# Performance work log

Hardware: AMD Instinct MI355X
Metric: run time of the kernel (lower is better)

## Reference

```python
import jax, jax.numpy as jnp
import numpy as np

WS = 4           # window size (cubic)
NUM_HEADS = 4
DIM = 128
NW = 392         # number of windows per sample
B = 8            # batch
N = WS ** 3      # 64 tokens per window


def _relative_position_index(ws):
    coords = np.stack(np.meshgrid(np.arange(ws), np.arange(ws), np.arange(ws), indexing='ij'))  # [3,ws,ws,ws]
    flat = coords.reshape(3, -1)                      # [3, ws^3]
    rel = flat[:, :, None] - flat[:, None, :]         # [3, N, N]
    rel = rel.transpose(1, 2, 0).copy()               # [N, N, 3]
    rel += ws - 1
    rel[:, :, 0] *= (2 * ws - 1) ** 2
    rel[:, :, 1] *= (2 * ws - 1)
    return rel.sum(-1)                                # [N, N] int


def setup_inputs() -> dict:
    key = jax.random.key(0)
    ks = jax.random.split(key, 8)
    B_ = NW * B
    x = jax.random.normal(ks[0], (B_, N, DIM), dtype=jnp.float32)
    mask = jax.random.normal(ks[1], (NW, N, N), dtype=jnp.float32)
    # learned params
    qkv_w = jax.random.normal(ks[2], (3 * DIM, DIM), dtype=jnp.float32) * 0.02
    qkv_b = jnp.zeros((3 * DIM,), dtype=jnp.float32)
    proj_w = jax.random.normal(ks[3], (DIM, DIM), dtype=jnp.float32) * 0.02
    proj_b = jnp.zeros((DIM,), dtype=jnp.float32)
    tbl = jax.random.normal(ks[4], ((2 * WS - 1) ** 3, NUM_HEADS), dtype=jnp.float32) * 0.02
    rel_index = jnp.asarray(_relative_position_index(WS), dtype=jnp.int32)  # [N, N]
    return {"x": x, "mask": mask, "qkv_w": qkv_w, "qkv_b": qkv_b,
            "proj_w": proj_w, "proj_b": proj_b, "rpb_table": tbl,
            "rel_index": rel_index}


def reference(x, mask, qkv_w, qkv_b, proj_w, proj_b, rpb_table, rel_index):
    B_, N_, C = x.shape
    H = NUM_HEADS
    hd = C // H
    scale = hd ** (-0.5)
    # qkv projection: [B_, N, 3, H, hd] -> (3, B_, H, N, hd)
    qkv = (x @ qkv_w.T + qkv_b).reshape(B_, N_, 3, H, hd).transpose(2, 0, 3, 1, 4)
    q, k, v = qkv[0], qkv[1], qkv[2]
    attn = jnp.einsum('bhnd,bhmd->bhnm', q * scale, k)        # [B_, H, N, N]
    # gathered relative position bias: [N, N, H] -> [H, N, N]
    rpe = rpb_table[rel_index].transpose(2, 0, 1)
    attn = attn + rpe[None]
    nW = mask.shape[0]
    attn = attn.reshape(B_ // nW, nW, H, N_, N_) + mask[None, :, None]
    attn = attn.reshape(B_, H, N_, N_)
    attn = jax.nn.softmax(attn, axis=-1)
    out = jnp.einsum('bhnm,bhmd->bnhd', attn, v).reshape(B_, N_, C)
    return out @ proj_w.T + proj_b
```

## Files before the change

### kernel.cpp

```cpp
#include <hip/hip_runtime.h>
#include <hip/hip_bf16.h>


typedef __bf16 bf16x8 __attribute__((ext_vector_type(8)));
typedef __bf16 bf16x4 __attribute__((ext_vector_type(4)));
typedef float f32x4 __attribute__((ext_vector_type(4)));

#define NWMASK 392
#define SCALE 0.17677669529663687f

__global__ void prep(const float* __restrict__ qkv_w, const float* __restrict__ proj_w,
                     const float* __restrict__ tbl, const int* __restrict__ ridx,
                     __bf16* __restrict__ wqkv, __bf16* __restrict__ wproj,
                     float* __restrict__ rpe) {
    int i = blockIdx.x * 256 + threadIdx.x;
    if (i < 49152) {
        wqkv[i] = (__bf16)qkv_w[i];
    } else if (i < 65536) {
        int j = i - 49152;  wproj[j] = (__bf16)proj_w[j];
    } else {
        int j = i - 65536;
        rpe[j] = tbl[ridx[j & 4095] * 4 + (j >> 12)];
    }
}

__global__ __launch_bounds__(256, 4) void wattn_main(
    const float* __restrict__ x, const float* __restrict__ mask,
    const float* __restrict__ qkv_b, const float* __restrict__ proj_b,
    const __bf16* __restrict__ wqkv, const __bf16* __restrict__ wproj,
    const float* __restrict__ rpe, float* __restrict__ out)
{
    __shared__ __align__(16) __bf16 smem[18944];
    const int win  = blockIdx.x;
    const int tid  = threadIdx.x;
    const int h    = tid >> 6;
    const int lane = tid & 63;
    const int quad = lane >> 4;
    const int l16  = lane & 15;

    __bf16* const xs  = smem;
    __bf16* const buf = smem + 8704 + h * 2560;

    {
        const float* xb = x + (size_t)win * 8192;
        #pragma unroll
        for (int i = 0; i < 2; ++i) {
            const int row  = h * 16 + (lane >> 3) + i * 8;
            const int colg = (lane & 7) * 16;
            const float* xp = xb + row * 128 + colg;
            float4 a0 = *(const float4*)(xp);
            float4 a1 = *(const float4*)(xp + 4);
            float4 a2 = *(const float4*)(xp + 8);
            float4 a3 = *(const float4*)(xp + 12);
            bf16x8 t0, t1;
            t0[0]=(__bf16)a0.x; t0[1]=(__bf16)a0.y; t0[2]=(__bf16)a0.z; t0[3]=(__bf16)a0.w;
            t0[4]=(__bf16)a1.x; t0[5]=(__bf16)a1.y; t0[6]=(__bf16)a1.z; t0[7]=(__bf16)a1.w;
            t1[0]=(__bf16)a2.x; t1[1]=(__bf16)a2.y; t1[2]=(__bf16)a2.z; t1[3]=(__bf16)a2.w;
            t1[4]=(__bf16)a3.x; t1[5]=(__bf16)a3.y; t1[6]=(__bf16)a3.z; t1[7]=(__bf16)a3.w;
            *(bf16x8*)(xs + row * 136 + colg)     = t0;
            *(bf16x8*)(xs + row * 136 + colg + 8) = t1;
        }
    }

    bf16x8 kwf[2][4]; float kbb[2];
    #pragma unroll
    for (int nt = 0; nt < 2; ++nt) {
        const int ng = 128 + h * 32 + nt * 16 + l16;
        kbb[nt] = qkv_b[ng];
        #pragma unroll
        for (int kt = 0; kt < 4; ++kt)
            kwf[nt][kt] = *(const bf16x8*)(wqkv + ng * 128 + kt * 32 + quad * 8);
    }
    __syncthreads();

    bf16x8 kf[4], qf[4], vf[2][2];

    {
        #pragma unroll
        for (int mt = 0; mt < 4; ++mt) {
            bf16x8 af[4];
            #pragma unroll
            for (int kt = 0; kt < 4; ++kt)
                af[kt] = *(const bf16x8*)(xs + (mt * 16 + l16) * 136 + kt * 32 + quad * 8);
            #pragma unroll
            for (int nt = 0; nt < 2; ++nt) {
                f32x4 acc = {0.f, 0.f, 0.f, 0.f};
                #pragma unroll
                for (int kt = 0; kt < 4; ++kt)
                    acc = __builtin_amdgcn_mfma_f32_16x16x32_bf16(af[kt], kwf[nt][kt], acc, 0, 0, 0);
                #pragma unroll
                for (int r = 0; r < 4; ++r)
                    buf[(mt * 16 + quad * 4 + r) * 40 + nt * 16 + l16] = (__bf16)(acc[r] + kbb[nt]);
            }
        }
        #pragma unroll
        for (int j = 0; j < 4; ++j)
            kf[j] = *(const bf16x8*)(buf + (j * 16 + l16) * 40 + quad * 8);
    }

    {
        bf16x8 wf[2][4]; float bb[2];
        #pragma unroll
        for (int nt = 0; nt < 2; ++nt) {
            const int ng = h * 32 + nt * 16 + l16;
            bb[nt] = qkv_b[ng];
            #pragma unroll
            for (int kt = 0; kt < 4; ++kt)
                wf[nt][kt] = *(const bf16x8*)(wqkv + ng * 128 + kt * 32 + quad * 8);
        }
        #pragma unroll
        for (int mt = 0; mt < 4; ++mt) {
            bf16x8 af[4];
            #pragma unroll
            for (int kt = 0; kt < 4; ++kt)
                af[kt] = *(const bf16x8*)(xs + (mt * 16 + l16) * 136 + kt * 32 + quad * 8);
            #pragma unroll
            for (int nt = 0; nt < 2; ++nt) {
                f32x4 acc = {0.f, 0.f, 0.f, 0.f};
                #pragma unroll
                for (int kt = 0; kt < 4; ++kt)
                    acc = __builtin_amdgcn_mfma_f32_16x16x32_bf16(af[kt], wf[nt][kt], acc, 0, 0, 0);
                #pragma unroll
                for (int r = 0; r < 4; ++r)
                    buf[(mt * 16 + quad * 4 + r) * 40 + nt * 16 + l16] = (__bf16)((acc[r] + bb[nt]) * SCALE);
            }
        }
        #pragma unroll
        for (int mt = 0; mt < 4; ++mt)
            qf[mt] = *(const bf16x8*)(buf + (mt * 16 + l16) * 40 + quad * 8);
    }

    {
        bf16x8 wf[2][4]; float bb[2];
        #pragma unroll
        for (int nt = 0; nt < 2; ++nt) {
            const int ng = 256 + h * 32 + nt * 16 + l16;
            bb[nt] = qkv_b[ng];
            #pragma unroll
            for (int kt = 0; kt < 4; ++kt)
                wf[nt][kt] = *(const bf16x8*)(wqkv + ng * 128 + kt * 32 + quad * 8);
        }
        #pragma unroll
        for (int mt = 0; mt < 4; ++mt) {
            bf16x8 af[4];
            #pragma unroll
            for (int kt = 0; kt < 4; ++kt)
                af[kt] = *(const bf16x8*)(xs + (mt * 16 + l16) * 136 + kt * 32 + quad * 8);
            #pragma unroll
            for (int nt = 0; nt < 2; ++nt) {
                f32x4 acc = {0.f, 0.f, 0.f, 0.f};
                #pragma unroll
                for (int kt = 0; kt < 4; ++kt)
                    acc = __builtin_amdgcn_mfma_f32_16x16x32_bf16(af[kt], wf[nt][kt], acc, 0, 0, 0);
                bf16x4 pk;
                #pragma unroll
                for (int r = 0; r < 4; ++r) pk[r] = (__bf16)(acc[r] + bb[nt]);
                *(bf16x4*)(buf + (nt * 16 + l16) * 72 + mt * 16 + quad * 4) = pk;
            }
        }
        #pragma unroll
        for (int kt = 0; kt < 2; ++kt)
            #pragma unroll
            for (int nf = 0; nf < 2; ++nf)
                vf[kt][nf] = *(const bf16x8*)(buf + (nf * 16 + l16) * 72 + kt * 32 + quad * 8);
    }
    __syncthreads();

    bf16x8 onesf;
    #pragma unroll
    for (int j = 0; j < 8; ++j) onesf[j] = (__bf16)1.0f;

    const float* rpeh = rpe + h * 4096;
    const float* mw   = mask + (size_t)(win % NWMASK) * 4096;
    #pragma unroll
    for (int mt = 0; mt < 4; ++mt) {
        float rb[4][4], mb[4][4];
        #pragma unroll
        for (int nt = 0; nt < 4; ++nt)
            #pragma unroll
            for (int r = 0; r < 4; ++r) {
                const int row = mt * 16 + quad * 4 + r;
                rb[nt][r] = rpeh[row * 64 + nt * 16 + l16];
                mb[nt][r] = mw[row * 64 + nt * 16 + l16];
            }
        f32x4 sc[4];
        #pragma unroll
        for (int nt = 0; nt < 4; ++nt) {
            f32x4 z = {0.f, 0.f, 0.f, 0.f};
            sc[nt] = __builtin_amdgcn_mfma_f32_16x16x32_bf16(qf[mt], kf[nt], z, 0, 0, 0);
        }
        #pragma unroll
        for (int nt = 0; nt < 4; ++nt)
            #pragma unroll
            for (int r = 0; r < 4; ++r)
                buf[(quad * 4 + r) * 72 + nt * 16 + l16] =
                    (__bf16)__expf(sc[nt][r] + rb[nt][r] + mb[nt][r]);
        f32x4 oa[2] = {{0.f,0.f,0.f,0.f},{0.f,0.f,0.f,0.f}};
        f32x4 os = {0.f, 0.f, 0.f, 0.f};
        #pragma unroll
        for (int kt = 0; kt < 2; ++kt) {
            bf16x8 pf = *(const bf16x8*)(buf + l16 * 72 + kt * 32 + quad * 8);
            oa[0] = __builtin_amdgcn_mfma_f32_16x16x32_bf16(pf, vf[kt][0], oa[0], 0, 0, 0);
            oa[1] = __builtin_amdgcn_mfma_f32_16x16x32_bf16(pf, vf[kt][1], oa[1], 0, 0, 0);
            os    = __builtin_amdgcn_mfma_f32_16x16x32_bf16(pf, onesf,     os,    0, 0, 0);
        }
        #pragma unroll
        for (int r = 0; r < 4; ++r) {
            const float inv = 1.0f / os[r];
            const int orow = mt * 16 + quad * 4 + r;
            xs[orow * 136 + h * 32 + l16]      = (__bf16)(oa[0][r] * inv);
            xs[orow * 136 + h * 32 + 16 + l16] = (__bf16)(oa[1][r] * inv);
        }
    }
    __syncthreads();

    bf16x8 of[4];
    #pragma unroll
    for (int kt = 0; kt < 4; ++kt)
        of[kt] = *(const bf16x8*)(xs + (h * 16 + l16) * 136 + kt * 32 + quad * 8);
    #pragma unroll
    for (int nt = 0; nt < 8; ++nt) {
        const int ng = nt * 16 + l16;
        const float b = proj_b[ng];
        bf16x8 wf[4];
        #pragma unroll
        for (int kt = 0; kt < 4; ++kt)
            wf[kt] = *(const bf16x8*)(wproj + ng * 128 + kt * 32 + quad * 8);
        f32x4 acc = {0.f, 0.f, 0.f, 0.f};
        #pragma unroll
        for (int kt = 0; kt < 4; ++kt)
            acc = __builtin_amdgcn_mfma_f32_16x16x32_bf16(of[kt], wf[kt], acc, 0, 0, 0);
        float* dst = out + ((size_t)win * 64 + h * 16 + quad * 4) * 128 + ng;
        #pragma unroll
        for (int r = 0; r < 4; ++r) dst[(size_t)r * 128] = acc[r] + b;
    }
}

extern "C" void kernel_launch(void* const* d_in, const int* in_sizes, int n_in,
                              void* d_out, int out_size, void* d_ws, size_t ws_size,
                              hipStream_t stream) {
    const float* x      = (const float*)d_in[0];
    const float* mask   = (const float*)d_in[1];
    const float* qkv_w  = (const float*)d_in[2];
    const float* qkv_b  = (const float*)d_in[3];
    const float* proj_w = (const float*)d_in[4];
    const float* proj_b = (const float*)d_in[5];
    const float* tbl    = (const float*)d_in[6];
    const int*   ridx   = (const int*)d_in[7];
    float* out = (float*)d_out;

    __bf16* wqkv  = (__bf16*)d_ws;
    __bf16* wproj = wqkv + 384 * 128;
    float*  rpe   = (float*)((char*)d_ws + 131072);

    prep<<<320, 256, 0, stream>>>(qkv_w, proj_w, tbl, ridx, wqkv, wproj, rpe);
    wattn_main<<<3136, 256, 0, stream>>>(x, mask, qkv_b, proj_b, wqkv, wproj, rpe, out);
}
```

Before: 270.2 us.

## Transpose rpe/mask in prep, swap MFMA operands, halve per-wave LDS buffer

The prep kernel now writes the relative position bias transposed and, when workspace allows, also a transposed copy of the mask. This lets the main kernel load bias and mask as f32x4 vectors that match the MFMA output layout, prefetched one row tile ahead instead of issuing scalar gathers. Q/K projections swap MFMA operand order so results are stored as packed bf16x4. Q, K and V are staged through LDS in two halves, which halves the per-wave buffer and the total shared memory. This adds extra prep work (transposing the mask each call) and a fallback template path.

Measured after the change: 301.8 us. 11.7% more time.

```diff
diff --git a/kernel.cpp b/kernel.cpp
--- a/kernel.cpp
+++ b/kernel.cpp
@@ -12,25 +12,42 @@
 __global__ void prep(const float* __restrict__ qkv_w, const float* __restrict__ proj_w,
                      const float* __restrict__ tbl, const int* __restrict__ ridx,
                      __bf16* __restrict__ wqkv, __bf16* __restrict__ wproj,
-                     float* __restrict__ rpe) {
-    int i = blockIdx.x * 256 + threadIdx.x;
-    if (i < 49152) {
-        wqkv[i] = (__bf16)qkv_w[i];
-    } else if (i < 65536) {
-        int j = i - 49152;  wproj[j] = (__bf16)proj_w[j];
+                     float* __restrict__ rpe_t,
+                     const float* __restrict__ mask, float* __restrict__ mask_t,
+                     int do_mask) {
+    __shared__ float t[64][65];
+    if (blockIdx.x < 320) {
+        int i = blockIdx.x * 256 + threadIdx.x;
+        if (i < 49152) {
+            wqkv[i] = (__bf16)qkv_w[i];
+        } else if (i < 65536) {
+            int j = i - 49152;  wproj[j] = (__bf16)proj_w[j];
+        } else {
+            int j = i - 65536;
+            rpe_t[j] = tbl[ridx[(j & 63) * 64 + ((j >> 6) & 63)] * 4 + (j >> 12)];
+        }
     } else {
-        int j = i - 65536;
-        rpe[j] = tbl[ridx[j & 4095] * 4 + (j >> 12)];
+        if (!do_mask) return;
+        const int w = blockIdx.x - 320;
+        const int c = threadIdx.x & 63, rb = threadIdx.x >> 6;
+        const float* src = mask + (size_t)w * 4096;
+        #pragma unroll
+        for (int i = 0; i < 16; ++i) { int r = rb * 16 + i; t[r][c] = src[r * 64 + c]; }
+        __syncthreads();
+        float* dst = mask_t + (size_t)w * 4096;
+        #pragma unroll
+        for (int i = 0; i < 16; ++i) { int r = rb * 16 + i; dst[r * 64 + c] = t[c][r]; }
     }
 }
 
+template<bool TB>
 __global__ __launch_bounds__(256, 4) void wattn_main(
-    const float* __restrict__ x, const float* __restrict__ mask,
+    const float* __restrict__ x, const float* __restrict__ maskp,
     const float* __restrict__ qkv_b, const float* __restrict__ proj_b,
     const __bf16* __restrict__ wqkv, const __bf16* __restrict__ wproj,
-    const float* __restrict__ rpe, float* __restrict__ out)
+    const float* __restrict__ rpe_t, float* __restrict__ out)
 {
-    __shared__ __align__(16) __bf16 smem[18944];
+    __shared__ __align__(16) __bf16 smem[13824];
     const int win  = blockIdx.x;
     const int tid  = threadIdx.x;
     const int h    = tid >> 6;
@@ -39,7 +56,7 @@
     const int l16  = lane & 15;
 
     __bf16* const xs  = smem;
-    __bf16* const buf = smem + 8704 + h * 2560;
+    __bf16* const buf = smem + 8704 + h * 1280;
 
     {
         const float* xb = x + (size_t)win * 8192;
@@ -62,11 +79,11 @@
         }
     }
 
-    bf16x8 kwf[2][4]; float kbb[2];
+    bf16x8 kwf[2][4]; f32x4 kb4[2];
     #pragma unroll
     for (int nt = 0; nt < 2; ++nt) {
         const int ng = 128 + h * 32 + nt * 16 + l16;
-        kbb[nt] = qkv_b[ng];
+        kb4[nt] = *(const f32x4*)(qkv_b + 128 + h * 32 + nt * 16 + quad * 4);
         #pragma unroll
         for (int kt = 0; kt < 4; ++kt)
             kwf[nt][kt] = *(const bf16x8*)(wqkv + ng * 128 + kt * 32 + quad * 8);
@@ -75,9 +92,11 @@
 
     bf16x8 kf[4], qf[4], vf[2][2];
 
-    {
-        #pragma unroll
-        for (int mt = 0; mt < 4; ++mt) {
+    #pragma unroll
+    for (int half = 0; half < 2; ++half) {
+        #pragma unroll
+        for (int m2 = 0; m2 < 2; ++m2) {
+            const int mt = half * 2 + m2;
             bf16x8 af[4];
             #pragma unroll
             for (int kt = 0; kt < 4; ++kt)
@@ -87,82 +106,99 @@
                 f32x4 acc = {0.f, 0.f, 0.f, 0.f};
                 #pragma unroll
                 for (int kt = 0; kt < 4; ++kt)
-                    acc = __builtin_amdgcn_mfma_f32_16x16x32_bf16(af[kt], kwf[nt][kt], acc, 0, 0, 0);
-                #pragma unroll
-                for (int r = 0; r < 4; ++r)
-                    buf[(mt * 16 + quad * 4 + r) * 40 + nt * 16 + l16] = (__bf16)(acc[r] + kbb[nt]);
-            }
-        }
-        #pragma unroll
-        for (int j = 0; j < 4; ++j)
-            kf[j] = *(const bf16x8*)(buf + (j * 16 + l16) * 40 + quad * 8);
+                    acc = __builtin_amdgcn_mfma_f32_16x16x32_bf16(kwf[nt][kt], af[kt], acc, 0, 0, 0);
+                bf16x4 pk;
+                #pragma unroll
+                for (int r = 0; r < 4; ++r) pk[r] = (__bf16)(acc[r] + kb4[nt][r]);
+                *(bf16x4*)(buf + (m2 * 16 + l16) * 40 + nt * 16 + quad * 4) = pk;
+            }
+        }
+        kf[half * 2 + 0] = *(const bf16x8*)(buf + l16 * 40 + quad * 8);
+        kf[half * 2 + 1] = *(const bf16x8*)(buf + (16 + l16) * 40 + quad * 8);
     }
 
     {
-        bf16x8 wf[2][4]; float bb[2];
+        bf16x8 qwf[2][4]; f32x4 qb4[2];
         #pragma unroll
         for (int nt = 0; nt < 2; ++nt) {
             const int ng = h * 32 + nt * 16 + l16;
-            bb[nt] = qkv_b[ng];
+            qb4[nt] = *(const f32x4*)(qkv_b + h * 32 + nt * 16 + quad * 4);
             #pragma unroll
             for (int kt = 0; kt < 4; ++kt)
-                wf[nt][kt] = *(const bf16x8*)(wqkv + ng * 128 + kt * 32 + quad * 8);
-        }
-        #pragma unroll
-        for (int mt = 0; mt < 4; ++mt) {
-            bf16x8 af[4];
-            #pragma unroll
-            for (int kt = 0; kt < 4; ++kt)
-                af[kt] = *(const bf16x8*)(xs + (mt * 16 + l16) * 136 + kt * 32 + quad * 8);
-            #pragma unroll
-            for (int nt = 0; nt < 2; ++nt) {
-                f32x4 acc = {0.f, 0.f, 0.f, 0.f};
+                qwf[nt][kt] = *(const bf16x8*)(wqkv + ng * 128 + kt * 32 + quad * 8);
+        }
+        #pragma unroll
+        for (int half = 0; half < 2; ++half) {
+            #pragma unroll
+            for (int m2 = 0; m2 < 2; ++m2) {
+                const int mt = half * 2 + m2;
+                bf16x8 af[4];
                 #pragma unroll
                 for (int kt = 0; kt < 4; ++kt)
-                    acc = __builtin_amdgcn_mfma_f32_16x16x32_bf16(af[kt], wf[nt][kt], acc, 0, 0, 0);
-                #pragma unroll
-                for (int r = 0; r < 4; ++r)
-                    buf[(mt * 16 + quad * 4 + r) * 40 + nt * 16 + l16] = (__bf16)((acc[r] + bb[nt]) * SCALE);
-            }
-        }
-        #pragma unroll
-        for (int mt = 0; mt < 4; ++mt)
-            qf[mt] = *(const bf16x8*)(buf + (mt * 16 + l16) * 40 + quad * 8);
+                    af[kt] = *(const bf16x8*)(xs + (mt * 16 + l16) * 136 + kt * 32 + quad * 8);
+                #pragma unroll
+                for (int nt = 0; nt < 2; ++nt) {
+                    f32x4 acc = {0.f, 0.f, 0.f, 0.f};
+                    #pragma unroll
+                    for (int kt = 0; kt < 4; ++kt)
+                        acc = __builtin_amdgcn_mfma_f32_16x16x32_bf16(qwf[nt][kt], af[kt], acc, 0, 0, 0);
+                    bf16x4 pk;
+                    #pragma unroll
+                    for (int r = 0; r < 4; ++r) pk[r] = (__bf16)((acc[r] + qb4[nt][r]) * SCALE);
+                    *(bf16x4*)(buf + (m2 * 16 + l16) * 40 + nt * 16 + quad * 4) = pk;
+                }
+            }
+            qf[half * 2 + 0] = *(const bf16x8*)(buf + l16 * 40 + quad * 8);
+            qf[half * 2 + 1] = *(const bf16x8*)(buf + (16 + l16) * 40 + quad * 8);
+        }
     }
 
     {
-        bf16x8 wf[2][4]; float bb[2];
+        bf16x8 vwf[2][4]; float vbb[2];
         #pragma unroll
         for (int nt = 0; nt < 2; ++nt) {
             const int ng = 256 + h * 32 + nt * 16 + l16;
-            bb[nt] = qkv_b[ng];
+            vbb[nt] = qkv_b[ng];
             #pragma unroll
             for (int kt = 0; kt < 4; ++kt)
-                wf[nt][kt] = *(const bf16x8*)(wqkv + ng * 128 + kt * 32 + quad * 8);
-        }
-        #pragma unroll
-        for (int mt = 0; mt < 4; ++mt) {
-            bf16x8 af[4];
-            #pragma unroll
-            for (int kt = 0; kt < 4; ++kt)
-                af[kt] = *(const bf16x8*)(xs + (mt * 16 + l16) * 136 + kt * 32 + quad * 8);
-            #pragma unroll
-            for (int nt = 0; nt < 2; ++nt) {
-                f32x4 acc = {0.f, 0.f, 0.f, 0.f};
+                vwf[nt][kt] = *(const bf16x8*)(wqkv + ng * 128 + kt * 32 + quad * 8);
+        }
+        #pragma unroll
+        for (int half = 0; half < 2; ++half) {
+            #pragma unroll
+            for (int m2 = 0; m2 < 2; ++m2) {
+                const int mt = half * 2 + m2;
+                bf16x8 af[4];
                 #pragma unroll
                 for (int kt = 0; kt < 4; ++kt)
-                    acc = __builtin_amdgcn_mfma_f32_16x16x32_bf16(af[kt], wf[nt][kt], acc, 0, 0, 0);
-                bf16x4 pk;
-                #pragma unroll
-                for (int r = 0; r < 4; ++r) pk[r] = (__bf16)(acc[r] + bb[nt]);
-                *(bf16x4*)(buf + (nt * 16 + l16) * 72 + mt * 16 + quad * 4) = pk;
-            }
-        }
-        #pragma unroll
-        for (int kt = 0; kt < 2; ++kt)
+                    af[kt] = *(const bf16x8*)(xs + (mt * 16 + l16) * 136 + kt * 32 + quad * 8);
+                #pragma unroll
+                for (int nt = 0; nt < 2; ++nt) {
+                    f32x4 acc = {0.f, 0.f, 0.f, 0.f};
+                    #pragma unroll
+                    for (int kt = 0; kt < 4; ++kt)
+                        acc = __builtin_amdgcn_mfma_f32_16x16x32_bf16(af[kt], vwf[nt][kt], acc, 0, 0, 0);
+                    bf16x4 pk;
+                    #pragma unroll
+                    for (int r = 0; r < 4; ++r) pk[r] = (__bf16)(acc[r] + vbb[nt]);
+                    *(bf16x4*)(buf + (nt * 16 + l16) * 40 + m2 * 16 + quad * 4) = pk;
+                }
+            }
             #pragma unroll
             for (int nf = 0; nf < 2; ++nf)
-                vf[kt][nf] = *(const bf16x8*)(buf + (nf * 16 + l16) * 72 + kt * 32 + quad * 8);
+                vf[half][nf] = *(const bf16x8*)(buf + (nf * 16 + l16) * 40 + quad * 8);
+        }
+    }
+
+    const int wm = win % NWMASK;
+    const float* rt = rpe_t + h * 4096;
+    const float* mw = maskp + (size_t)wm * 4096;
+    f32x4 rb4[4], mb4[4];
+    #pragma unroll
+    for (int nt = 0; nt < 4; ++nt) {
+        rb4[nt] = *(const f32x4*)(rt + (nt * 16 + l16) * 64 + quad * 4);
+        if constexpr (TB)
+            mb4[nt] = *(const f32x4*)(mw + (nt * 16 + l16) * 64 + quad * 4);
     }
     __syncthreads();
 
@@ -170,31 +206,38 @@
     #pragma unroll
     for (int j = 0; j < 8; ++j) onesf[j] = (__bf16)1.0f;
 
-    const float* rpeh = rpe + h * 4096;
-    const float* mw   = mask + (size_t)(win % NWMASK) * 4096;
     #pragma unroll
     for (int mt = 0; mt < 4; ++mt) {
-        float rb[4][4], mb[4][4];
-        #pragma unroll
-        for (int nt = 0; nt < 4; ++nt)
-            #pragma unroll
-            for (int r = 0; r < 4; ++r) {
-                const int row = mt * 16 + quad * 4 + r;
-                rb[nt][r] = rpeh[row * 64 + nt * 16 + l16];
-                mb[nt][r] = mw[row * 64 + nt * 16 + l16];
-            }
         f32x4 sc[4];
         #pragma unroll
         for (int nt = 0; nt < 4; ++nt) {
             f32x4 z = {0.f, 0.f, 0.f, 0.f};
             sc[nt] = __builtin_amdgcn_mfma_f32_16x16x32_bf16(qf[mt], kf[nt], z, 0, 0, 0);
         }
+        float mbs[4][4];
+        if constexpr (!TB) {
+            #pragma unroll
+            for (int nt = 0; nt < 4; ++nt)
+                #pragma unroll
+                for (int r = 0; r < 4; ++r)
+                    mbs[nt][r] = mw[(mt * 16 + quad * 4 + r) * 64 + nt * 16 + l16];
+        }
         #pragma unroll
         for (int nt = 0; nt < 4; ++nt)
             #pragma unroll
-            for (int r = 0; r < 4; ++r)
+            for (int r = 0; r < 4; ++r) {
+                const float m = TB ? mb4[nt][r] : mbs[nt][r];
                 buf[(quad * 4 + r) * 72 + nt * 16 + l16] =
-                    (__bf16)__expf(sc[nt][r] + rb[nt][r] + mb[nt][r]);
+                    (__bf16)__expf(sc[nt][r] + rb4[nt][r] + m);
+            }
+        if (mt < 3) {
+            #pragma unroll
+            for (int nt = 0; nt < 4; ++nt) {
+                rb4[nt] = *(const f32x4*)(rt + (nt * 16 + l16) * 64 + (mt + 1) * 16 + quad * 4);
+                if constexpr (TB)
+                    mb4[nt] = *(const f32x4*)(mw + (nt * 16 + l16) * 64 + (mt + 1) * 16 + quad * 4);
+            }
+        }
         f32x4 oa[2] = {{0.f,0.f,0.f,0.f},{0.f,0.f,0.f,0.f}};
         f32x4 os = {0.f, 0.f, 0.f, 0.f};
         #pragma unroll
@@ -251,8 +294,18 @@
 
     __bf16* wqkv  = (__bf16*)d_ws;
     __bf16* wproj = wqkv + 384 * 128;
-    float*  rpe   = (float*)((char*)d_ws + 131072);
-
-    prep<<<320, 256, 0, stream>>>(qkv_w, proj_w, tbl, ridx, wqkv, wproj, rpe);
-    wattn_main<<<3136, 256, 0, stream>>>(x, mask, qkv_b, proj_b, wqkv, wproj, rpe, out);
+    float*  rpe_t = (float*)((char*)d_ws + 131072);
+    float*  mask_t = (float*)((char*)d_ws + 196608);
+    const size_t need_tb = 196608 + (size_t)NWMASK * 4096 * 4;
+    const bool tb = ws_size >= need_tb;
+
+    prep<<<tb ? 712 : 320, 256, 0, stream>>>(qkv_w, proj_w, tbl, ridx,
+                                             wqkv, wproj, rpe_t, mask, mask_t,
+                                             tb ? 1 : 0);
+    if (tb)
+        wattn_main<true><<<3136, 256, 0, stream>>>(x, mask_t, qkv_b, proj_b,
+                                                   wqkv, wproj, rpe_t, out);
+    else
+        wattn_main<false><<<3136, 256, 0, stream>>>(x, mask, qkv_b, proj_b,
+                                                    wqkv, wproj, rpe_t, out);
 }
```
